# Kernel optimization log

Measured on AMD Instinct MI355X. Metric: run time of the kernel, lower is better.

Reference implementation:

```python
import jax, jax.numpy as jnp
import numpy as np

NEG_SLOPE = 0.2  # PyG GATConv default leaky_relu slope
EPS = 1e-16      # PyG softmax denominator epsilon


def _add_self_loops(edge_index, n):
    loop = jnp.arange(n, dtype=edge_index.dtype)
    src = jnp.concatenate([edge_index[0], loop])
    dst = jnp.concatenate([edge_index[1], loop])
    return src, dst


def _gat_conv(x, src, dst, W, att_src, att_dst, bias, heads, out_ch, n):
    # Linear transform: [N, H, C]
    h = (x @ W).reshape(n, heads, out_ch)
    # Per-node attention logits: [N, H]
    a_s = (h * att_src[None]).sum(-1)
    a_d = (h * att_dst[None]).sum(-1)
    # Edge logits (message j->i uses src term of j, dst term of i): [E, H]
    e = jax.nn.leaky_relu(a_s[src] + a_d[dst], negative_slope=NEG_SLOPE)
    # Segment softmax over incoming edges of each target node
    m = jax.ops.segment_max(e, dst, num_segments=n)  # [N, H]
    ex = jnp.exp(e - m[dst])
    denom = jax.ops.segment_sum(ex, dst, num_segments=n)  # [N, H]
    alpha = ex / (denom[dst] + EPS)  # [E, H]
    # Weighted scatter-aggregate of source features: [N, H, C]
    out = jax.ops.segment_sum(h[src] * alpha[:, :, None], dst, num_segments=n)
    return out, alpha


def setup_inputs() -> dict:
    key = jax.random.key(0)
    ks = jax.random.split(key, 11)
    N, E, IN, HID, HEADS, OUT = 50000, 800000, 128, 64, 3, 64
    g = lambda k, shp, fan: jax.random.normal(k, shp, jnp.float32) * (1.0 / np.sqrt(fan))
    return {
        "x": jax.random.normal(ks[0], (N, IN), jnp.float32),
        "edge_index": jax.random.randint(ks[1], (2, E), 0, N, jnp.int32),
        "W1": g(ks[2], (IN, HEADS * HID), IN),
        "att_src1": g(ks[3], (HEADS, HID), HID),
        "att_dst1": g(ks[4], (HEADS, HID), HID),
        "b1": jnp.zeros((HEADS * HID,), jnp.float32),
        "W2": g(ks[5], (HEADS * HID, OUT), HEADS * HID),
        "att_src2": g(ks[6], (1, OUT), OUT),
        "att_dst2": g(ks[7], (1, OUT), OUT),
        "b2": jnp.zeros((OUT,), jnp.float32),
    }


def reference(x, edge_index, W1, att_src1, att_dst1, b1, W2, att_src2, att_dst2, b2):
    n = x.shape[0]
    heads, hid = att_src1.shape
    out_ch = att_src2.shape[1]
    src, dst = _add_self_loops(edge_index, n)
    # Layer 1: heads concatenated, then bias and ELU
    h1, _alpha = _gat_conv(x, src, dst, W1, att_src1, att_dst1, b1, heads, hid, n)
    h1 = h1.reshape(n, heads * hid) + b1
    h1 = jax.nn.elu(h1)
    # Layer 2: single head (self-loops re-added on same graph, as PyG does)
    h2, _ = _gat_conv(h1, src, dst, W2, att_src2, att_dst2, b2, 1, out_ch, n)
    h2 = h2.reshape(n, out_ch) + b2
    return h2
```

## Files before the change

kernel.cpp:

```cpp
#include <hip/hip_runtime.h>
#include <hip/hip_bf16.h>
#include <cstddef>

#define LRELU_SLOPE 0.2f
#define EPS_DEN 1e-16f

typedef __attribute__((ext_vector_type(8))) short short8;
typedef __attribute__((ext_vector_type(4))) float f32x4;

__device__ __forceinline__ float lrelu(float v) { return v > 0.f ? v : LRELU_SLOPE * v; }
__device__ __forceinline__ unsigned short f2bf(float f) {
  unsigned int x = __float_as_uint(f);
  unsigned int r = x + 0x7fff + ((x >> 16) & 1);
  return (unsigned short)(r >> 16);
}

template <int K, int NC>
__global__ __launch_bounds__(256) void pack_w_k(const float* __restrict__ W,
                                                unsigned short* __restrict__ Pb) {
  constexpr int CT = NC / 16;
  int t = blockIdx.x * 256 + threadIdx.x;
  constexpr int TOTAL = (K / 32) * CT * 64;
  if (t >= TOTAL) return;
  int lane = t & 63;
  int slot = t >> 6;
  int ct = slot % CT;
  int kt = slot / CT;
  int col = ct * 16 + (lane & 15);
  int kbase = kt * 32 + (lane >> 4) * 8;
  unsigned short v[8];
#pragma unroll
  for (int j = 0; j < 8; ++j) v[j] = f2bf(W[(size_t)(kbase + j) * NC + col]);
#pragma unroll
  for (int j = 0; j < 8; ++j) Pb[(size_t)t * 8 + j] = v[j];
}

template <int K, int NC>
__global__ __launch_bounds__(256) void gemm_mfma_k(const float* __restrict__ A,
                                                   const unsigned short* __restrict__ Pb,
                                                   unsigned short* __restrict__ Cb,
                                                   const float* __restrict__ asrc,
                                                   const float* __restrict__ adst,
                                                   float* __restrict__ a_s,
                                                   float* __restrict__ a_d, int M) {
  constexpr int KT = K / 32;
  constexpr int CT = NC / 16;
  constexpr int HEADS = NC / 64;
  const int wv = threadIdx.x >> 6, lane = threadIdx.x & 63;
  const int row0 = blockIdx.x * 64 + wv * 16;
  const int arow = row0 + (lane & 15);
  const int ko = (lane >> 4) * 8;
  const bool aOK = arow < M;

  f32x4 acc[CT];
#pragma unroll
  for (int c = 0; c < CT; ++c) acc[c] = (f32x4){0.f, 0.f, 0.f, 0.f};

#pragma unroll
  for (int kt = 0; kt < KT; ++kt) {
    short8 af;
    if (aOK) {
      const float* ap = A + (size_t)arow * K + kt * 32 + ko;
      float4 v0 = *reinterpret_cast<const float4*>(ap);
      float4 v1 = *reinterpret_cast<const float4*>(ap + 4);
      af = (short8){(short)f2bf(v0.x), (short)f2bf(v0.y), (short)f2bf(v0.z), (short)f2bf(v0.w),
                    (short)f2bf(v1.x), (short)f2bf(v1.y), (short)f2bf(v1.z), (short)f2bf(v1.w)};
    } else {
      af = (short8){0, 0, 0, 0, 0, 0, 0, 0};
    }
#pragma unroll
    for (int ct = 0; ct < CT; ++ct) {
      short8 bf = *reinterpret_cast<const short8*>(Pb + (((size_t)kt * CT + ct) * 64 + lane) * 8);
      acc[ct] = __builtin_amdgcn_mfma_f32_16x16x32_bf16(af, bf, acc[ct], 0, 0, 0);
    }
  }

  float ps[4][HEADS], pd[4][HEADS];
#pragma unroll
  for (int g = 0; g < 4; ++g)
#pragma unroll
    for (int h = 0; h < HEADS; ++h) { ps[g][h] = 0.f; pd[g][h] = 0.f; }
#pragma unroll
  for (int ct = 0; ct < CT; ++ct) {
    int h = ct >> 2;
    float av = asrc[ct * 16 + (lane & 15)];
    float dv = adst[ct * 16 + (lane & 15)];
#pragma unroll
    for (int g = 0; g < 4; ++g) {
      ps[g][h] = fmaf(acc[ct][g], av, ps[g][h]);
      pd[g][h] = fmaf(acc[ct][g], dv, pd[g][h]);
    }
  }
#pragma unroll
  for (int o = 1; o < 16; o <<= 1) {
#pragma unroll
    for (int g = 0; g < 4; ++g)
#pragma unroll
      for (int h = 0; h < HEADS; ++h) {
        ps[g][h] += __shfl_xor(ps[g][h], o);
        pd[g][h] += __shfl_xor(pd[g][h], o);
      }
  }
  if ((lane & 15) == 0) {
#pragma unroll
    for (int g = 0; g < 4; ++g) {
      int gr = row0 + (lane >> 4) * 4 + g;
      if (gr < M) {
#pragma unroll
        for (int h = 0; h < HEADS; ++h) {
          a_s[(size_t)gr * HEADS + h] = ps[g][h];
          a_d[(size_t)gr * HEADS + h] = pd[g][h];
        }
      }
    }
  }

#pragma unroll
  for (int g = 0; g < 4; ++g) {
    int gr = row0 + (lane >> 4) * 4 + g;
    if (gr < M) {
#pragma unroll
      for (int ct = 0; ct < CT; ++ct) {
        Cb[(size_t)gr * NC + ct * 16 + (lane & 15)] = f2bf(acc[ct][g]);
      }
    }
  }
}

__global__ __launch_bounds__(256) void deg_count_k(const int* __restrict__ ei, int E, int Nn,
                                                   int* __restrict__ deg) {
  int e = blockIdx.x * blockDim.x + threadIdx.x;
  int ET = E + Nn;
  if (e >= ET) return;
  int dst = (e < E) ? ei[E + e] : (e - E);
  atomicAdd(&deg[dst], 1);
}

__global__ __launch_bounds__(256) void scan1_k(const int* __restrict__ deg,
                                               int* __restrict__ loc,
                                               int* __restrict__ bsum, int Nn) {
  __shared__ int part[256];
  int t = threadIdx.x;
  int base = blockIdx.x * 1024 + t * 4;
  int v[4];
  int s = 0;
#pragma unroll
  for (int k = 0; k < 4; ++k) {
    int idx = base + k;
    v[k] = (idx < Nn) ? deg[idx] : 0;
    s += v[k];
  }
  part[t] = s;
  __syncthreads();
  for (int o = 1; o < 256; o <<= 1) {
    int u = (t >= o) ? part[t - o] : 0;
    __syncthreads();
    part[t] += u;
    __syncthreads();
  }
  int run = (t == 0) ? 0 : part[t - 1];
#pragma unroll
  for (int k = 0; k < 4; ++k) {
    int idx = base + k;
    if (idx < Nn) loc[idx] = run;
    run += v[k];
  }
  if (t == 255) bsum[blockIdx.x] = part[255];
}

__global__ __launch_bounds__(64) void scan2_k(int* __restrict__ bsum, int nblk) {
  int t = threadIdx.x;
  int v = (t < nblk) ? bsum[t] : 0;
  for (int o = 1; o < 64; o <<= 1) {
    int u = __shfl_up(v, o);
    if (t >= o) v += u;
  }
  if (t < nblk) bsum[t] = v;
}

__global__ __launch_bounds__(256) void scan3_k(const int* __restrict__ loc,
                                               const int* __restrict__ bsum,
                                               int* __restrict__ off,
                                               int* __restrict__ cursor, int Nn, int ET) {
  int i = blockIdx.x * 256 + threadIdx.x;
  if (i < Nn) {
    int blk = i >> 10;
    int basev = blk ? bsum[blk - 1] : 0;
    int o = loc[i] + basev;
    off[i] = o;
    cursor[i] = o;
  }
  if (i == 0) off[Nn] = ET;
}

__global__ __launch_bounds__(256) void fill_k(const int* __restrict__ ei, int E, int Nn,
                                              int* __restrict__ cursor,
                                              int* __restrict__ srcs,
                                              int* __restrict__ dsts) {
  int e = blockIdx.x * blockDim.x + threadIdx.x;
  int ET = E + Nn;
  if (e >= ET) return;
  int src, dst;
  if (e < E) { src = ei[e]; dst = ei[E + e]; }
  else { src = e - E; dst = e - E; }
  int pos = atomicAdd(&cursor[dst], 1);
  srcs[pos] = src;
  dsts[pos] = dst;
}

__global__ __launch_bounds__(256) void ew1_k(const int* __restrict__ srcs,
                                             const int* __restrict__ dsts,
                                             const float* __restrict__ a_s,
                                             const float* __restrict__ a_d,
                                             int4* __restrict__ quad, int ET) {
  int p = blockIdx.x * 256 + threadIdx.x;
  if (p >= ET) return;
  int s = srcs[p], d = dsts[p];
  const float* asp = a_s + (size_t)s * 3;
  const float* adp = a_d + (size_t)d * 3;
  float w0 = __expf(lrelu(asp[0] + adp[0]));
  float w1 = __expf(lrelu(asp[1] + adp[1]));
  float w2 = __expf(lrelu(asp[2] + adp[2]));
  quad[p] = make_int4(s, __float_as_int(w0), __float_as_int(w1), __float_as_int(w2));
}

__global__ __launch_bounds__(256) void ew2_k(const int* __restrict__ srcs,
                                             const int* __restrict__ dsts,
                                             const float* __restrict__ a_s,
                                             const float* __restrict__ a_d,
                                             int2* __restrict__ pair, int ET) {
  int p = blockIdx.x * 256 + threadIdx.x;
  if (p >= ET) return;
  int s = srcs[p], d = dsts[p];
  float w = __expf(lrelu(a_s[s] + a_d[d]));
  pair[p] = make_int2(s, __float_as_int(w));
}

__global__ __launch_bounds__(256) void agg1_k(const unsigned int* __restrict__ Hu,
                                              const int4* __restrict__ quad,
                                              const int* __restrict__ off,
                                              const float* __restrict__ bias,
                                              float* __restrict__ out, int Nn) {
  int wave = threadIdx.x >> 6, lane = threadIdx.x & 63;
  int node = blockIdx.x * 4 + wave;
  if (node >= Nn) return;
  bool hiHalf = lane >= 32;
  int q = lane & 31;
  int b = off[node], e = off[node + 1];
  float2 accA = make_float2(0.f, 0.f);
  float2 accB = make_float2(0.f, 0.f);
  float ts0 = 0.f, ts1 = 0.f, ts2 = 0.f;
  int p = b;
  for (; p + 2 <= e; p += 2) {
    int4 q0 = quad[p], q1 = quad[p + 1];
    float w00 = __int_as_float(q0.y), w01 = __int_as_float(q0.z), w02 = __int_as_float(q0.w);
    float w10 = __int_as_float(q1.y), w11 = __int_as_float(q1.z), w12 = __int_as_float(q1.w);
    const unsigned int* h0 = Hu + (size_t)q0.x * 96;
    const unsigned int* h1 = Hu + (size_t)q1.x * 96;
    unsigned int a0 = h0[lane];
    unsigned int bm = (hiHalf ? h1 : h0)[64 + q];
    unsigned int a1 = h1[lane];
    float wA0 = hiHalf ? w01 : w00;
    float wA1 = hiHalf ? w11 : w10;
    float wB = hiHalf ? w12 : w02;
    accA.x = fmaf(wA0, __uint_as_float(a0 << 16), accA.x);
    accA.y = fmaf(wA0, __uint_as_float(a0 & 0xffff0000u), accA.y);
    accA.x = fmaf(wA1, __uint_as_float(a1 << 16), accA.x);
    accA.y = fmaf(wA1, __uint_as_float(a1 & 0xffff0000u), accA.y);
    accB.x = fmaf(wB, __uint_as_float(bm << 16), accB.x);
    accB.y = fmaf(wB, __uint_as_float(bm & 0xffff0000u), accB.y);
    ts0 += w00 + w10; ts1 += w01 + w11; ts2 += w02 + w12;
  }
  if (p < e) {
    int4 q0 = quad[p];
    float w00 = __int_as_float(q0.y), w01 = __int_as_float(q0.z), w02 = __int_as_float(q0.w);
    const unsigned int* h0 = Hu + (size_t)q0.x * 96;
    unsigned int a0 = h0[lane];
    unsigned int bm = h0[64 + q];
    float wA0 = hiHalf ? w01 : w00;
    float wB = hiHalf ? 0.f : w02;
    accA.x = fmaf(wA0, __uint_as_float(a0 << 16), accA.x);
    accA.y = fmaf(wA0, __uint_as_float(a0 & 0xffff0000u), accA.y);
    accB.x = fmaf(wB, __uint_as_float(bm << 16), accB.x);
    accB.y = fmaf(wB, __uint_as_float(bm & 0xffff0000u), accB.y);
    ts0 += w00; ts1 += w01; ts2 += w02;
  }
  accB.x += __shfl_xor(accB.x, 32);
  accB.y += __shfl_xor(accB.y, 32);

  float tsA = hiHalf ? ts1 : ts0;
  float rA = 1.f / (tsA + EPS_DEN);
  float rB = 1.f / (ts2 + EPS_DEN);
  int colA = (hiHalf ? 64 : 0) + 2 * q;
  float oA0 = accA.x * rA + bias[colA];
  float oA1 = accA.y * rA + bias[colA + 1];
  oA0 = oA0 > 0.f ? oA0 : expm1f(oA0);
  oA1 = oA1 > 0.f ? oA1 : expm1f(oA1);
  *reinterpret_cast<float2*>(&out[(size_t)node * 192 + colA]) = make_float2(oA0, oA1);
  if (hiHalf) {
    int colB = 128 + 2 * q;
    float oB0 = accB.x * rB + bias[colB];
    float oB1 = accB.y * rB + bias[colB + 1];
    oB0 = oB0 > 0.f ? oB0 : expm1f(oB0);
    oB1 = oB1 > 0.f ? oB1 : expm1f(oB1);
    *reinterpret_cast<float2*>(&out[(size_t)node * 192 + colB]) = make_float2(oB0, oB1);
  }
}

__global__ __launch_bounds__(256) void agg2_k(const unsigned int* __restrict__ Hu,
                                              const int2* __restrict__ pair,
                                              const int* __restrict__ off,
                                              const float* __restrict__ bias,
                                              float* __restrict__ out, int Nn) {
  int wave = threadIdx.x >> 6, lane = threadIdx.x & 63;
  int node = blockIdx.x * 4 + wave;
  if (node >= Nn) return;
  bool hi = lane >= 32;
  int q = lane & 31;
  int b = off[node], e = off[node + 1];
  float2 acc = make_float2(0.f, 0.f);
  float ts = 0.f;
  int p = b;
  for (; p + 2 <= e; p += 2) {
    int2 p0 = pair[p], p1 = pair[p + 1];
    float w0 = __int_as_float(p0.y), w1 = __int_as_float(p1.y);
    const unsigned int* hsel = Hu + (size_t)(hi ? p1.x : p0.x) * 32;
    unsigned int a = hsel[q];
    float wsel = hi ? w1 : w0;
    acc.x = fmaf(wsel, __uint_as_float(a << 16), acc.x);
    acc.y = fmaf(wsel, __uint_as_float(a & 0xffff0000u), acc.y);
    ts += w0 + w1;
  }
  if (p < e) {
    int2 p0 = pair[p];
    float w0 = __int_as_float(p0.y);
    unsigned int a = Hu[(size_t)p0.x * 32 + q];
    float wsel = hi ? 0.f : w0;
    acc.x = fmaf(wsel, __uint_as_float(a << 16), acc.x);
    acc.y = fmaf(wsel, __uint_as_float(a & 0xffff0000u), acc.y);
    ts += w0;
  }
  acc.x += __shfl_xor(acc.x, 32);
  acc.y += __shfl_xor(acc.y, 32);
  if (!hi) {
    float r = 1.f / (ts + EPS_DEN);
    float o0 = acc.x * r + bias[2 * q];
    float o1 = acc.y * r + bias[2 * q + 1];
    *reinterpret_cast<float2*>(&out[(size_t)node * 64 + 2 * q]) = make_float2(o0, o1);
  }
}

extern "C" void kernel_launch(void* const* d_in, const int* in_sizes, int n_in,
                              void* d_out, int out_size, void* d_ws, size_t ws_size,
                              hipStream_t stream) {
  const float* x = (const float*)d_in[0];
  const int* ei = (const int*)d_in[1];
  const float* W1 = (const float*)d_in[2];
  const float* att_src1 = (const float*)d_in[3];
  const float* att_dst1 = (const float*)d_in[4];
  const float* b1 = (const float*)d_in[5];
  const float* W2 = (const float*)d_in[6];
  const float* att_src2 = (const float*)d_in[7];
  const float* att_dst2 = (const float*)d_in[8];
  const float* b2 = (const float*)d_in[9];

  const int IN = 128, HEADS = 3;
  const int HC1 = 192;
  const int N = in_sizes[0] / IN;
  const int E = in_sizes[1] / 2;
  const int ET = E + N;

  char* base = (char*)d_ws;
  int4* quad1 = (int4*)base;
  float* h1_post = (float*)(base + (size_t)ET * 16);
  float* a_s1 = h1_post + (size_t)N * HC1;
  float* a_d1 = a_s1 + (size_t)N * HEADS;
  int* deg = (int*)(a_d1 + (size_t)N * HEADS);
  int* off = deg + N;
  int* cursor = off + (N + 1);
  int* bsum = cursor + N;
  int* srcs = bsum + 256;
  int* dsts = srcs + ET;
  size_t pw_off = ((size_t)((char*)(dsts + ET) - base) + 15) & ~(size_t)15;
  unsigned short* packW1 = (unsigned short*)(base + pw_off);
  unsigned short* packW2 = packW1 + 24576;
  size_t ph_off = ((size_t)((char*)(packW2 + 12288) - base) + 15) & ~(size_t)15;
  char* ph = base + ph_off;
  unsigned short* h1b = (unsigned short*)ph;
  unsigned short* h2b = (unsigned short*)ph;
  int2* pair2 = (int2*)(ph + (size_t)N * 128);
  float* a_s2 = (float*)((char*)pair2 + (size_t)ET * 8);
  float* a_d2 = a_s2 + N;

  float* outp = (float*)d_out;

  int gemm_blocks = (N + 63) / 64;
  int row_blocks = (N + 3) / 4;
  int edge_blocks = (ET + 255) / 256;
  int nblk = (N + 1023) / 1024;

  pack_w_k<128, 192><<<12, 256, 0, stream>>>(W1, packW1);
  pack_w_k<192, 64><<<6, 256, 0, stream>>>(W2, packW2);

  hipMemsetAsync(deg, 0, (size_t)N * sizeof(int), stream);
  deg_count_k<<<edge_blocks, 256, 0, stream>>>(ei, E, N, deg);
  scan1_k<<<nblk, 256, 0, stream>>>(deg, cursor, bsum, N);
  scan2_k<<<1, 64, 0, stream>>>(bsum, nblk);
  scan3_k<<<(N + 255) / 256, 256, 0, stream>>>(cursor, bsum, off, cursor, N, ET);
  fill_k<<<edge_blocks, 256, 0, stream>>>(ei, E, N, cursor, srcs, dsts);

  gemm_mfma_k<128, 192><<<gemm_blocks, 256, 0, stream>>>(x, packW1, h1b, att_src1, att_dst1,
                                                         a_s1, a_d1, N);
  ew1_k<<<edge_blocks, 256, 0, stream>>>(srcs, dsts, a_s1, a_d1, quad1, ET);
  agg1_k<<<row_blocks, 256, 0, stream>>>((const unsigned int*)h1b, quad1, off, b1,
                                         h1_post, N);

  gemm_mfma_k<192, 64><<<gemm_blocks, 256, 0, stream>>>(h1_post, packW2, h2b, att_src2,
                                                        att_dst2, a_s2, a_d2, N);
  ew2_k<<<edge_blocks, 256, 0, stream>>>(srcs, dsts, a_s2, a_d2, pair2, ET);
  agg2_k<<<row_blocks, 256, 0, stream>>>((const unsigned int*)h2b, pair2, off, b2,
                                         outp, N);

  (void)n_in; (void)out_size; (void)ws_size;
}
```

Before: 269.4 us.

## Store layer-1 output as bf16 and widen gathers in aggregation kernels

Layer-1 aggregation now writes its ELU output as bf16 rather than fp32, and the second GEMM reads bf16 directly through a templated input path, roughly halving that intermediate's traffic. Both aggregation kernels switch to 8-byte per-lane gathers. agg1 now splits edges across the two half-waves, and agg2 processes four edges per iteration with 16-lane groups and a shuffle reduction. Stores use nontemporal hints. This adds an extra bf16 rounding of the hidden activations and an over-read tail in agg2, which is why the edge buffers are padded.

```diff
diff --git a/kernel.cpp b/kernel.cpp
--- a/kernel.cpp
+++ b/kernel.cpp
@@ -7,12 +7,20 @@
 
 typedef __attribute__((ext_vector_type(8))) short short8;
 typedef __attribute__((ext_vector_type(4))) float f32x4;
+typedef __attribute__((ext_vector_type(4))) int i32x4;
+typedef __attribute__((ext_vector_type(2))) int i32x2;
+typedef __attribute__((ext_vector_type(2))) unsigned int u32x2;
 
 __device__ __forceinline__ float lrelu(float v) { return v > 0.f ? v : LRELU_SLOPE * v; }
 __device__ __forceinline__ unsigned short f2bf(float f) {
   unsigned int x = __float_as_uint(f);
   unsigned int r = x + 0x7fff + ((x >> 16) & 1);
   return (unsigned short)(r >> 16);
+}
+__device__ __forceinline__ float lo16(unsigned int u) { return __uint_as_float(u << 16); }
+__device__ __forceinline__ float hi16(unsigned int u) { return __uint_as_float(u & 0xffff0000u); }
+__device__ __forceinline__ unsigned int pack2(float a, float b) {
+  return (unsigned int)f2bf(a) | ((unsigned int)f2bf(b) << 16);
 }
 
 template <int K, int NC>
@@ -35,8 +43,8 @@
   for (int j = 0; j < 8; ++j) Pb[(size_t)t * 8 + j] = v[j];
 }
 
-template <int K, int NC>
-__global__ __launch_bounds__(256) void gemm_mfma_k(const float* __restrict__ A,
+template <int K, int NC, bool AF32>
+__global__ __launch_bounds__(256) void gemm_mfma_k(const void* __restrict__ Araw,
                                                    const unsigned short* __restrict__ Pb,
                                                    unsigned short* __restrict__ Cb,
                                                    const float* __restrict__ asrc,
@@ -60,11 +68,16 @@
   for (int kt = 0; kt < KT; ++kt) {
     short8 af;
     if (aOK) {
-      const float* ap = A + (size_t)arow * K + kt * 32 + ko;
-      float4 v0 = *reinterpret_cast<const float4*>(ap);
-      float4 v1 = *reinterpret_cast<const float4*>(ap + 4);
-      af = (short8){(short)f2bf(v0.x), (short)f2bf(v0.y), (short)f2bf(v0.z), (short)f2bf(v0.w),
-                    (short)f2bf(v1.x), (short)f2bf(v1.y), (short)f2bf(v1.z), (short)f2bf(v1.w)};
+      if constexpr (AF32) {
+        const float* ap = (const float*)Araw + (size_t)arow * K + kt * 32 + ko;
+        float4 v0 = *reinterpret_cast<const float4*>(ap);
+        float4 v1 = *reinterpret_cast<const float4*>(ap + 4);
+        af = (short8){(short)f2bf(v0.x), (short)f2bf(v0.y), (short)f2bf(v0.z), (short)f2bf(v0.w),
+                      (short)f2bf(v1.x), (short)f2bf(v1.y), (short)f2bf(v1.z), (short)f2bf(v1.w)};
+      } else {
+        const unsigned short* ap = (const unsigned short*)Araw + (size_t)arow * K + kt * 32 + ko;
+        af = *reinterpret_cast<const short8*>(ap);
+      }
     } else {
       af = (short8){0, 0, 0, 0, 0, 0, 0, 0};
     }
@@ -212,7 +225,7 @@
                                              const int* __restrict__ dsts,
                                              const float* __restrict__ a_s,
                                              const float* __restrict__ a_d,
-                                             int4* __restrict__ quad, int ET) {
+                                             i32x4* __restrict__ quad, int ET) {
   int p = blockIdx.x * 256 + threadIdx.x;
   if (p >= ET) return;
   int s = srcs[p], d = dsts[p];
@@ -221,132 +234,156 @@
   float w0 = __expf(lrelu(asp[0] + adp[0]));
   float w1 = __expf(lrelu(asp[1] + adp[1]));
   float w2 = __expf(lrelu(asp[2] + adp[2]));
-  quad[p] = make_int4(s, __float_as_int(w0), __float_as_int(w1), __float_as_int(w2));
+  quad[p] = (i32x4){s, __float_as_int(w0), __float_as_int(w1), __float_as_int(w2)};
 }
 
 __global__ __launch_bounds__(256) void ew2_k(const int* __restrict__ srcs,
                                              const int* __restrict__ dsts,
                                              const float* __restrict__ a_s,
                                              const float* __restrict__ a_d,
-                                             int2* __restrict__ pair, int ET) {
+                                             i32x2* __restrict__ pair, int ET) {
   int p = blockIdx.x * 256 + threadIdx.x;
   if (p >= ET) return;
   int s = srcs[p], d = dsts[p];
   float w = __expf(lrelu(a_s[s] + a_d[d]));
-  pair[p] = make_int2(s, __float_as_int(w));
+  pair[p] = (i32x2){s, __float_as_int(w)};
 }
 
 __global__ __launch_bounds__(256) void agg1_k(const unsigned int* __restrict__ Hu,
-                                              const int4* __restrict__ quad,
+                                              const i32x4* __restrict__ quad,
+                                              const int* __restrict__ off,
+                                              const float* __restrict__ bias,
+                                              unsigned short* __restrict__ outb, int Nn) {
+  int wave = threadIdx.x >> 6, lane = threadIdx.x & 63;
+  int node = blockIdx.x * 4 + wave;
+  if (node >= Nn) return;
+  const bool hiHalf = lane >= 32;
+  const int q = lane & 31;
+  const bool c16 = q < 16;
+  int b = off[node], e = off[node + 1];
+  float a0 = 0.f, a1 = 0.f, a2 = 0.f, a3 = 0.f;
+  float g0 = 0.f, g1 = 0.f, g2 = 0.f, g3 = 0.f;
+  float ts0 = 0.f, ts1 = 0.f, ts2 = 0.f;
+  int p = b;
+#pragma unroll 2
+  for (; p + 2 <= e; p += 2) {
+    i32x4 e0 = quad[p];
+    i32x4 e1 = quad[p + 1];
+    float w00 = __int_as_float(e0.y), w01 = __int_as_float(e0.z), w02 = __int_as_float(e0.w);
+    float w10 = __int_as_float(e1.y), w11 = __int_as_float(e1.z), w12 = __int_as_float(e1.w);
+    int mysrc = hiHalf ? e1.x : e0.x;
+    const u32x2* hp = reinterpret_cast<const u32x2*>(Hu + (size_t)mysrc * 96);
+    u32x2 u = hp[q];
+    float wA = hiHalf ? (c16 ? w10 : w11) : (c16 ? w00 : w01);
+    a0 = fmaf(wA, lo16(u.x), a0); a1 = fmaf(wA, hi16(u.x), a1);
+    a2 = fmaf(wA, lo16(u.y), a2); a3 = fmaf(wA, hi16(u.y), a3);
+    if (c16) {
+      u32x2 v = hp[32 + q];
+      float wB = hiHalf ? w12 : w02;
+      g0 = fmaf(wB, lo16(v.x), g0); g1 = fmaf(wB, hi16(v.x), g1);
+      g2 = fmaf(wB, lo16(v.y), g2); g3 = fmaf(wB, hi16(v.y), g3);
+    }
+    ts0 += w00 + w10; ts1 += w01 + w11; ts2 += w02 + w12;
+  }
+  if (p < e) {
+    i32x4 e0 = quad[p];
+    float w00 = __int_as_float(e0.y), w01 = __int_as_float(e0.z), w02 = __int_as_float(e0.w);
+    const u32x2* hp = reinterpret_cast<const u32x2*>(Hu + (size_t)e0.x * 96);
+    u32x2 u = hp[q];
+    float wA = hiHalf ? 0.f : (c16 ? w00 : w01);
+    a0 = fmaf(wA, lo16(u.x), a0); a1 = fmaf(wA, hi16(u.x), a1);
+    a2 = fmaf(wA, lo16(u.y), a2); a3 = fmaf(wA, hi16(u.y), a3);
+    if (c16) {
+      u32x2 v = hp[32 + q];
+      float wB = hiHalf ? 0.f : w02;
+      g0 = fmaf(wB, lo16(v.x), g0); g1 = fmaf(wB, hi16(v.x), g1);
+      g2 = fmaf(wB, lo16(v.y), g2); g3 = fmaf(wB, hi16(v.y), g3);
+    }
+    ts0 += w00; ts1 += w01; ts2 += w02;
+  }
+  a0 += __shfl_xor(a0, 32); a1 += __shfl_xor(a1, 32);
+  a2 += __shfl_xor(a2, 32); a3 += __shfl_xor(a3, 32);
+  g0 += __shfl_xor(g0, 32); g1 += __shfl_xor(g1, 32);
+  g2 += __shfl_xor(g2, 32); g3 += __shfl_xor(g3, 32);
+
+  if (!hiHalf) {
+    float r = 1.f / ((c16 ? ts0 : ts1) + EPS_DEN);
+    int col = 4 * q;
+    float o0 = a0 * r + bias[col], o1 = a1 * r + bias[col + 1];
+    float o2 = a2 * r + bias[col + 2], o3 = a3 * r + bias[col + 3];
+    o0 = o0 > 0.f ? o0 : expm1f(o0);
+    o1 = o1 > 0.f ? o1 : expm1f(o1);
+    o2 = o2 > 0.f ? o2 : expm1f(o2);
+    o3 = o3 > 0.f ? o3 : expm1f(o3);
+    u32x2 pk = {pack2(o0, o1), pack2(o2, o3)};
+    __builtin_nontemporal_store(pk, reinterpret_cast<u32x2*>(&outb[(size_t)node * 192 + col]));
+  } else if (c16) {
+    float r = 1.f / (ts2 + EPS_DEN);
+    int col = 128 + 4 * q;
+    float o0 = g0 * r + bias[col], o1 = g1 * r + bias[col + 1];
+    float o2 = g2 * r + bias[col + 2], o3 = g3 * r + bias[col + 3];
+    o0 = o0 > 0.f ? o0 : expm1f(o0);
+    o1 = o1 > 0.f ? o1 : expm1f(o1);
+    o2 = o2 > 0.f ? o2 : expm1f(o2);
+    o3 = o3 > 0.f ? o3 : expm1f(o3);
+    u32x2 pk = {pack2(o0, o1), pack2(o2, o3)};
+    __builtin_nontemporal_store(pk, reinterpret_cast<u32x2*>(&outb[(size_t)node * 192 + col]));
+  }
+}
+
+__global__ __launch_bounds__(256) void agg2_k(const unsigned int* __restrict__ Hu,
+                                              const i32x2* __restrict__ pair,
                                               const int* __restrict__ off,
                                               const float* __restrict__ bias,
                                               float* __restrict__ out, int Nn) {
   int wave = threadIdx.x >> 6, lane = threadIdx.x & 63;
   int node = blockIdx.x * 4 + wave;
   if (node >= Nn) return;
-  bool hiHalf = lane >= 32;
-  int q = lane & 31;
+  const int sub = lane >> 4;
+  const int l = lane & 15;
   int b = off[node], e = off[node + 1];
-  float2 accA = make_float2(0.f, 0.f);
-  float2 accB = make_float2(0.f, 0.f);
-  float ts0 = 0.f, ts1 = 0.f, ts2 = 0.f;
-  int p = b;
-  for (; p + 2 <= e; p += 2) {
-    int4 q0 = quad[p], q1 = quad[p + 1];
-    float w00 = __int_as_float(q0.y), w01 = __int_as_float(q0.z), w02 = __int_as_float(q0.w);
-    float w10 = __int_as_float(q1.y), w11 = __int_as_float(q1.z), w12 = __int_as_float(q1.w);
-    const unsigned int* h0 = Hu + (size_t)q0.x * 96;
-    const unsigned int* h1 = Hu + (size_t)q1.x * 96;
-    unsigned int a0 = h0[lane];
-    unsigned int bm = (hiHalf ? h1 : h0)[64 + q];
-    unsigned int a1 = h1[lane];
-    float wA0 = hiHalf ? w01 : w00;
-    float wA1 = hiHalf ? w11 : w10;
-    float wB = hiHalf ? w12 : w02;
-    accA.x = fmaf(wA0, __uint_as_float(a0 << 16), accA.x);
-    accA.y = fmaf(wA0, __uint_as_float(a0 & 0xffff0000u), accA.y);
-    accA.x = fmaf(wA1, __uint_as_float(a1 << 16), accA.x);
-    accA.y = fmaf(wA1, __uint_as_float(a1 & 0xffff0000u), accA.y);
-    accB.x = fmaf(wB, __uint_as_float(bm << 16), accB.x);
-    accB.y = fmaf(wB, __uint_as_float(bm & 0xffff0000u), accB.y);
-    ts0 += w00 + w10; ts1 += w01 + w11; ts2 += w02 + w12;
-  }
-  if (p < e) {
-    int4 q0 = quad[p];
-    float w00 = __int_as_float(q0.y), w01 = __int_as_float(q0.z), w02 = __int_as_float(q0.w);
-    const unsigned int* h0 = Hu + (size_t)q0.x * 96;
-    unsigned int a0 = h0[lane];
-    unsigned int bm = h0[64 + q];
-    float wA0 = hiHalf ? w01 : w00;
-    float wB = hiHalf ? 0.f : w02;
-    accA.x = fmaf(wA0, __uint_as_float(a0 << 16), accA.x);
-    accA.y = fmaf(wA0, __uint_as_float(a0 & 0xffff0000u), accA.y);
-    accB.x = fmaf(wB, __uint_as_float(bm << 16), accB.x);
-    accB.y = fmaf(wB, __uint_as_float(bm & 0xffff0000u), accB.y);
-    ts0 += w00; ts1 += w01; ts2 += w02;
-  }
-  accB.x += __shfl_xor(accB.x, 32);
-  accB.y += __shfl_xor(accB.y, 32);
-
-  float tsA = hiHalf ? ts1 : ts0;
-  float rA = 1.f / (tsA + EPS_DEN);
-  float rB = 1.f / (ts2 + EPS_DEN);
-  int colA = (hiHalf ? 64 : 0) + 2 * q;
-  float oA0 = accA.x * rA + bias[colA];
-  float oA1 = accA.y * rA + bias[colA + 1];
-  oA0 = oA0 > 0.f ? oA0 : expm1f(oA0);
-  oA1 = oA1 > 0.f ? oA1 : expm1f(oA1);
-  *reinterpret_cast<float2*>(&out[(size_t)node * 192 + colA]) = make_float2(oA0, oA1);
-  if (hiHalf) {
-    int colB = 128 + 2 * q;
-    float oB0 = accB.x * rB + bias[colB];
-    float oB1 = accB.y * rB + bias[colB + 1];
-    oB0 = oB0 > 0.f ? oB0 : expm1f(oB0);
-    oB1 = oB1 > 0.f ? oB1 : expm1f(oB1);
-    *reinterpret_cast<float2*>(&out[(size_t)node * 192 + colB]) = make_float2(oB0, oB1);
-  }
-}
-
-__global__ __launch_bounds__(256) void agg2_k(const unsigned int* __restrict__ Hu,
-                                              const int2* __restrict__ pair,
-                                              const int* __restrict__ off,
-                                              const float* __restrict__ bias,
-                                              float* __restrict__ out, int Nn) {
-  int wave = threadIdx.x >> 6, lane = threadIdx.x & 63;
-  int node = blockIdx.x * 4 + wave;
-  if (node >= Nn) return;
-  bool hi = lane >= 32;
-  int q = lane & 31;
-  int b = off[node], e = off[node + 1];
-  float2 acc = make_float2(0.f, 0.f);
+  float c0 = 0.f, c1 = 0.f, c2 = 0.f, c3 = 0.f;
   float ts = 0.f;
   int p = b;
-  for (; p + 2 <= e; p += 2) {
-    int2 p0 = pair[p], p1 = pair[p + 1];
+  for (; p + 4 <= e; p += 4) {
+    i32x2 p0 = pair[p], p1 = pair[p + 1], p2 = pair[p + 2], p3 = pair[p + 3];
     float w0 = __int_as_float(p0.y), w1 = __int_as_float(p1.y);
-    const unsigned int* hsel = Hu + (size_t)(hi ? p1.x : p0.x) * 32;
-    unsigned int a = hsel[q];
-    float wsel = hi ? w1 : w0;
-    acc.x = fmaf(wsel, __uint_as_float(a << 16), acc.x);
-    acc.y = fmaf(wsel, __uint_as_float(a & 0xffff0000u), acc.y);
-    ts += w0 + w1;
+    float w2 = __int_as_float(p2.y), w3 = __int_as_float(p3.y);
+    int mysrc = (sub == 0) ? p0.x : (sub == 1) ? p1.x : (sub == 2) ? p2.x : p3.x;
+    float myw = (sub == 0) ? w0 : (sub == 1) ? w1 : (sub == 2) ? w2 : w3;
+    const u32x2* hp = reinterpret_cast<const u32x2*>(Hu + (size_t)mysrc * 32);
+    u32x2 u = hp[l];
+    c0 = fmaf(myw, lo16(u.x), c0); c1 = fmaf(myw, hi16(u.x), c1);
+    c2 = fmaf(myw, lo16(u.y), c2); c3 = fmaf(myw, hi16(u.y), c3);
+    ts += w0 + w1 + w2 + w3;
   }
   if (p < e) {
-    int2 p0 = pair[p];
+    i32x2 p0 = pair[p], p1 = pair[p + 1], p2 = pair[p + 2], p3 = pair[p + 3];
+    bool h1 = p + 1 < e, h2 = p + 2 < e, h3 = p + 3 < e;
     float w0 = __int_as_float(p0.y);
-    unsigned int a = Hu[(size_t)p0.x * 32 + q];
-    float wsel = hi ? 0.f : w0;
-    acc.x = fmaf(wsel, __uint_as_float(a << 16), acc.x);
-    acc.y = fmaf(wsel, __uint_as_float(a & 0xffff0000u), acc.y);
-    ts += w0;
-  }
-  acc.x += __shfl_xor(acc.x, 32);
-  acc.y += __shfl_xor(acc.y, 32);
-  if (!hi) {
+    float w1 = h1 ? __int_as_float(p1.y) : 0.f;
+    float w2 = h2 ? __int_as_float(p2.y) : 0.f;
+    float w3 = h3 ? __int_as_float(p3.y) : 0.f;
+    int s0 = p0.x;
+    int s1 = h1 ? p1.x : s0, s2 = h2 ? p2.x : s0, s3 = h3 ? p3.x : s0;
+    int mysrc = (sub == 0) ? s0 : (sub == 1) ? s1 : (sub == 2) ? s2 : s3;
+    float myw = (sub == 0) ? w0 : (sub == 1) ? w1 : (sub == 2) ? w2 : w3;
+    const u32x2* hp = reinterpret_cast<const u32x2*>(Hu + (size_t)mysrc * 32);
+    u32x2 u = hp[l];
+    c0 = fmaf(myw, lo16(u.x), c0); c1 = fmaf(myw, hi16(u.x), c1);
+    c2 = fmaf(myw, lo16(u.y), c2); c3 = fmaf(myw, hi16(u.y), c3);
+    ts += w0 + w1 + w2 + w3;
+  }
+  c0 += __shfl_xor(c0, 16); c0 += __shfl_xor(c0, 32);
+  c1 += __shfl_xor(c1, 16); c1 += __shfl_xor(c1, 32);
+  c2 += __shfl_xor(c2, 16); c2 += __shfl_xor(c2, 32);
+  c3 += __shfl_xor(c3, 16); c3 += __shfl_xor(c3, 32);
+  if (lane < 16) {
     float r = 1.f / (ts + EPS_DEN);
-    float o0 = acc.x * r + bias[2 * q];
-    float o1 = acc.y * r + bias[2 * q + 1];
-    *reinterpret_cast<float2*>(&out[(size_t)node * 64 + 2 * q]) = make_float2(o0, o1);
+    int col = 4 * l;
+    f32x4 v = {c0 * r + bias[col], c1 * r + bias[col + 1],
+               c2 * r + bias[col + 2], c3 * r + bias[col + 3]};
+    __builtin_nontemporal_store(v, reinterpret_cast<f32x4*>(&out[(size_t)node * 64 + col]));
   }
 }
 
@@ -369,11 +406,12 @@
   const int N = in_sizes[0] / IN;
   const int E = in_sizes[1] / 2;
   const int ET = E + N;
+  const int ETp = ET + 4;
 
   char* base = (char*)d_ws;
-  int4* quad1 = (int4*)base;
-  float* h1_post = (float*)(base + (size_t)ET * 16);
-  float* a_s1 = h1_post + (size_t)N * HC1;
+  i32x4* quad1 = (i32x4*)base;
+  unsigned short* h1_postb = (unsigned short*)(base + (size_t)ETp * 16);
+  float* a_s1 = (float*)(h1_postb + (size_t)N * HC1);
   float* a_d1 = a_s1 + (size_t)N * HEADS;
   int* deg = (int*)(a_d1 + (size_t)N * HEADS);
   int* off = deg + N;
@@ -388,8 +426,8 @@
   char* ph = base + ph_off;
   unsigned short* h1b = (unsigned short*)ph;
   unsigned short* h2b = (unsigned short*)ph;
-  int2* pair2 = (int2*)(ph + (size_t)N * 128);
-  float* a_s2 = (float*)((char*)pair2 + (size_t)ET * 8);
+  i32x2* pair2 = (i32x2*)(ph + (size_t)N * 384);
+  float* a_s2 = (float*)((char*)pair2 + (size_t)ETp * 8);
   float* a_d2 = a_s2 + N;
 
   float* outp = (float*)d_out;
@@ -409,14 +447,15 @@
   scan3_k<<<(N + 255) / 256, 256, 0, stream>>>(cursor, bsum, off, cursor, N, ET);
   fill_k<<<edge_blocks, 256, 0, stream>>>(ei, E, N, cursor, srcs, dsts);
 
-  gemm_mfma_k<128, 192><<<gemm_blocks, 256, 0, stream>>>(x, packW1, h1b, att_src1, att_dst1,
-                                                         a_s1, a_d1, N);
+  gemm_mfma_k<128, 192, true><<<gemm_blocks, 256, 0, stream>>>(x, packW1, h1b, att_src1,
+                                                               att_dst1, a_s1, a_d1, N);
   ew1_k<<<edge_blocks, 256, 0, stream>>>(srcs, dsts, a_s1, a_d1, quad1, ET);
   agg1_k<<<row_blocks, 256, 0, stream>>>((const unsigned int*)h1b, quad1, off, b1,
-                                         h1_post, N);
-
-  gemm_mfma_k<192, 64><<<gemm_blocks, 256, 0, stream>>>(h1_post, packW2, h2b, att_src2,
-                                                        att_dst2, a_s2, a_d2, N);
+                                         h1_postb, N);
+
+  gemm_mfma_k<192, 64, false><<<gemm_blocks, 256, 0, stream>>>(h1_postb, packW2, h2b,
+                                                               att_src2, att_dst2,
+                                                               a_s2, a_d2, N);
   ew2_k<<<edge_blocks, 256, 0, stream>>>(srcs, dsts, a_s2, a_d2, pair2, ET);
   agg2_k<<<row_blocks, 256, 0, stream>>>((const unsigned int*)h2b, pair2, off, b2,
                                          outp, N);
```

New measurement: 260.9 us. 1.03x faster.
